# Performance work log

Hardware: AMD Instinct MI355X
Metric: run time of the kernel (lower is better)

## Reference

```python
import jax, jax.numpy as jnp
import numpy as np

B, T, DMODEL = 8, 1024, 1024
N_HEADS, DK, DV = 16, 64, 64
FF_INNER = 4096


def setup_inputs() -> dict:
    key = jax.random.key(0)
    ks = jax.random.split(key, 9)
    s = 0.02  # init scale so softmax logits stay sane
    return {
        "x": jax.random.normal(ks[0], (B, T, DMODEL), dtype=jnp.float32),
        "Wq": jax.random.normal(ks[1], (N_HEADS, DMODEL, DK), dtype=jnp.float32) * s,
        "Wk": jax.random.normal(ks[2], (N_HEADS, DMODEL, DK), dtype=jnp.float32) * s,
        "Wv": jax.random.normal(ks[3], (N_HEADS, DMODEL, DV), dtype=jnp.float32) * s,
        "Wo": jax.random.normal(ks[4], (DMODEL, DMODEL), dtype=jnp.float32) * s,
        "W1": jax.random.normal(ks[5], (FF_INNER, DMODEL), dtype=jnp.float32) * s,
        "b1": jax.random.normal(ks[6], (FF_INNER,), dtype=jnp.float32) * s,
        "W2": jax.random.normal(ks[7], (DMODEL, FF_INNER), dtype=jnp.float32) * s,
        "b2": jax.random.normal(ks[8], (DMODEL,), dtype=jnp.float32) * s,
    }


def _pseudo_norm(y):
    # Original: y - mean - std (unbiased std, torch default). NOT a real layernorm.
    mean = jnp.mean(y, axis=-1, keepdims=True)
    std = jnp.std(y, axis=-1, keepdims=True, ddof=1)
    return y - mean - std


def reference(x, Wq, Wk, Wv, Wo, W1, b1, W2, b2):
    dk = Wq.shape[-1]
    # per-head projections: (B,T,D) x (H,D,dk) -> (B,H,T,dk)
    WQ = jnp.einsum("btd,hdk->bhtk", x, Wq)
    WK = jnp.einsum("btd,hdk->bhtk", x, Wk)
    WV = jnp.einsum("btd,hdv->bhtv", x, Wv)
    scores = jnp.einsum("bhqk,bhsk->bhqs", WQ, WK) / np.sqrt(dk).astype(np.float32)
    # Faithful to original: softmax over dim=2, i.e. the QUERY axis of (B,H,Tq,Tk)
    attn = jax.nn.softmax(scores, axis=2)
    part = jnp.einsum("bhqs,bhsv->bhqv", attn, WV)  # (B,H,T,dv)
    # concat heads: (B,T,H*dv) == (B,T,dmodel)
    part = part.transpose(0, 2, 1, 3).reshape(part.shape[0], part.shape[2], -1)
    out1 = part @ Wo + x
    out1 = _pseudo_norm(out1)
    # FeedForward: Linear(dmodel->inner), relu, Linear(inner->dmodel)
    h = jnp.maximum(out1 @ W1.T + b1, 0.0)
    out2 = h @ W2.T + b2 + out1
    return _pseudo_norm(out2)
```

## Files before the change

kernel.cpp:

```cpp
#include <hip/hip_runtime.h>
#include <hip/hip_bf16.h>
#include <math.h>


#define B_ 8
#define T_ 1024
#define D_ 1024
#define H_ 16
#define DK_ 64
#define FF_ 4096
#define M_ (B_ * T_)

typedef unsigned short u16;
typedef __attribute__((ext_vector_type(8))) short bf16x8;
typedef __attribute__((ext_vector_type(4))) float f32x4;

#define QSZ 8388608ull

__device__ __forceinline__ float b2f(u16 u) {
  union { unsigned int i; float f; } x;
  x.i = ((unsigned int)u) << 16;
  return x.f;
}
__device__ __forceinline__ u16 f2b(float f) {
  __hip_bfloat16 h = __float2bfloat16(f);
  return *(u16*)&h;
}
__device__ __forceinline__ float fexp2(float x) {
#if __has_builtin(__builtin_amdgcn_exp2f)
  return __builtin_amdgcn_exp2f(x);
#else
  return exp2f(x);
#endif
}
#define C_QK 0.1803368801111244f

typedef __attribute__((address_space(1))) const void gas_void;
typedef __attribute__((address_space(3))) void las_void;
__device__ __forceinline__ void gload16(const void* g, void* l) {
  __builtin_amdgcn_global_load_lds((gas_void*)g, (las_void*)l, 16, 0, 0);
}

template <int EPI>
__global__ __launch_bounds__(256) void gemm16_k(
    const u16* __restrict__ A, const u16* __restrict__ Bt,
    int M, int N, int K, int lda, int ldb,
    float* __restrict__ C, int ldc, u16* __restrict__ Cb,
    const float* __restrict__ res, const float* __restrict__ bias) {
  __shared__ __align__(16) u16 As[2][128 * 32];
  __shared__ __align__(16) u16 Bs[2][128 * 32];

  const int tid = threadIdx.x;
  const int lane = tid & 63, wv = tid >> 6;
  const int m0 = blockIdx.y * 128, n0 = blockIdx.x * 128;
  const int wr = (wv >> 1) * 64, wc = (wv & 1) * 64;

  f32x4 acc[4][4];
#pragma unroll
  for (int i = 0; i < 4; ++i)
#pragma unroll
    for (int j = 0; j < 4; ++j) acc[i][j] = (f32x4){0.f, 0.f, 0.f, 0.f};

  const int srow = wv * 16 + (lane >> 2);
  const int scol = (lane & 3) * 8;
  const int fr = lane & 15, fk = (lane >> 4) * 8;

  const u16* gA0 = &A[(size_t)(m0 + srow) * lda + scol];
  const u16* gA1 = &A[(size_t)(m0 + srow + 64) * lda + scol];
  const u16* gB0 = &Bt[(size_t)(n0 + srow) * ldb + scol];
  const u16* gB1 = &Bt[(size_t)(n0 + srow + 64) * ldb + scol];

  gload16(gA0, &As[0][wv * 512]);
  gload16(gA1, &As[0][2048 + wv * 512]);
  gload16(gB0, &Bs[0][wv * 512]);
  gload16(gB1, &Bs[0][2048 + wv * 512]);
  __syncthreads();

  int cur = 0;
  for (int k0 = 0; k0 < K; k0 += 32) {
    if (k0 + 32 < K) {
      int nx = cur ^ 1, ko = k0 + 32;
      gload16(gA0 + ko, &As[nx][wv * 512]);
      gload16(gA1 + ko, &As[nx][2048 + wv * 512]);
      gload16(gB0 + ko, &Bs[nx][wv * 512]);
      gload16(gB1 + ko, &Bs[nx][2048 + wv * 512]);
    }
    bf16x8 af[4], bfr[4];
#pragma unroll
    for (int mi = 0; mi < 4; ++mi)
      af[mi] = *(const bf16x8*)&As[cur][(wr + mi * 16 + fr) * 32 + fk];
#pragma unroll
    for (int ni = 0; ni < 4; ++ni)
      bfr[ni] = *(const bf16x8*)&Bs[cur][(wc + ni * 16 + fr) * 32 + fk];
#pragma unroll
    for (int mi = 0; mi < 4; ++mi)
#pragma unroll
      for (int ni = 0; ni < 4; ++ni)
        acc[mi][ni] = __builtin_amdgcn_mfma_f32_16x16x32_bf16(
            af[mi], bfr[ni], acc[mi][ni], 0, 0, 0);
    __syncthreads();
    cur ^= 1;
  }

  const int fq = (lane >> 4) * 4;
#pragma unroll
  for (int mi = 0; mi < 4; ++mi) {
#pragma unroll
    for (int ni = 0; ni < 4; ++ni) {
      const int row = m0 + wr + mi * 16 + fq;
      const int col = n0 + wc + ni * 16 + fr;
      f32x4 v = acc[mi][ni];
      if (EPI == 6) {
        const int seg = col >> 10, cl = col & 1023;
        if (seg < 2) {
          u16* dst = Cb + (size_t)seg * QSZ;
#pragma unroll
          for (int r = 0; r < 4; ++r)
            dst[(size_t)(row + r) * 1024 + cl] = f2b(v[r]);
        } else {
          ushort4 w;
          w.x = f2b(v[0]); w.y = f2b(v[1]); w.z = f2b(v[2]); w.w = f2b(v[3]);
          size_t vidx = 2 * QSZ +
                        (((size_t)(row >> 10) * 16 + (cl >> 6)) * 64 +
                         (cl & 63)) * (size_t)T_ + (row & 1023);
          *(ushort4*)&Cb[vidx] = w;
        }
      } else {
#pragma unroll
        for (int r = 0; r < 4; ++r) {
          float val = v[r];
          size_t idx = (size_t)(row + r) * ldc + col;
          if (EPI == 1) {
            C[idx] = val + res[idx];
          } else if (EPI == 2) {
            Cb[idx] = f2b(fmaxf(val + bias[col], 0.f));
          } else if (EPI == 3) {
            C[idx] = val + bias[col] + res[idx];
          } else if (EPI == 4) {
            C[idx] = C[idx] + val;
          }
        }
      }
    }
  }
}

__global__ __launch_bounds__(256) void cvt_k(const float* __restrict__ in,
                                             u16* __restrict__ out, int n4) {
  int i = blockIdx.x * 256 + threadIdx.x;
  if (i >= n4) return;
  float4 v = *(const float4*)&in[(size_t)i * 4];
  ushort4 o;
  o.x = f2b(v.x); o.y = f2b(v.y); o.z = f2b(v.z); o.w = f2b(v.w);
  *(ushort4*)&out[(size_t)i * 4] = o;
}

__global__ __launch_bounds__(256) void tconv_k(const float* __restrict__ src,
                                               u16* __restrict__ dst, int R,
                                               int C) {
  __shared__ __align__(16) float t[32][33];
  const size_t bo = (size_t)blockIdx.z * R * C;
  const int r0 = blockIdx.y * 32, c0 = blockIdx.x * 32;
  const int tid = threadIdx.x;
  const int row = tid >> 3, c4 = (tid & 7) * 4;
  float4 v = *(const float4*)&src[bo + (size_t)(r0 + row) * C + c0 + c4];
  t[row][c4 + 0] = v.x; t[row][c4 + 1] = v.y;
  t[row][c4 + 2] = v.z; t[row][c4 + 3] = v.w;
  __syncthreads();
  ushort4 o;
  o.x = f2b(t[c4 + 0][row]); o.y = f2b(t[c4 + 1][row]);
  o.z = f2b(t[c4 + 2][row]); o.w = f2b(t[c4 + 3][row]);
  *(ushort4*)&dst[bo + (size_t)(c0 + row) * R + r0 + c4] = o;
}

__global__ __launch_bounds__(256) void attn_lsum_k(
    const u16* __restrict__ q, const u16* __restrict__ k,
    float* __restrict__ Lrcp) {
  __shared__ __align__(16) u16 Qs[128 * 64];
  __shared__ float Lsh[2][128];
  const int tid = threadIdx.x, lane = tid & 63, wv = tid >> 6;
  const int s0 = blockIdx.x * 128, h = blockIdx.y, b = blockIdx.z;
  const int bh = b * H_ + h;
  const u16* qbase = q + (size_t)b * T_ * D_ + h * DK_;
  const u16* kbase = k + (size_t)b * T_ * D_ + h * DK_;

  const int wr = (wv >> 1) * 64, wc = (wv & 1) * 64;
  const int fr = lane & 15, fs8 = (lane >> 4) * 8, fq = (lane >> 4) * 4;

  bf16x8 kf[4][2];
#pragma unroll
  for (int mi = 0; mi < 4; ++mi)
#pragma unroll
    for (int ks = 0; ks < 2; ++ks)
      kf[mi][ks] = *(const bf16x8*)&kbase[(size_t)(s0 + wr + mi * 16 + fr) * D_ +
                                          ks * 32 + fs8];

  float lrun[4][4];
#pragma unroll
  for (int mi = 0; mi < 4; ++mi)
#pragma unroll
    for (int r = 0; r < 4; ++r) lrun[mi][r] = 0.f;

  const int srow = wv * 8 + (lane >> 3);
  const int sscol = ((lane & 7) ^ ((lane >> 3) & 7)) * 8;

  for (int q0 = 0; q0 < T_; q0 += 128) {
    __syncthreads();
#pragma unroll
    for (int it = 0; it < 4; ++it)
      gload16(&qbase[(size_t)(q0 + it * 32 + srow) * D_ + sscol],
              &Qs[(it * 32 + wv * 8) * 64]);
    __syncthreads();

    f32x4 acc[4][4];
#pragma unroll
    for (int mi = 0; mi < 4; ++mi)
#pragma unroll
      for (int ni = 0; ni < 4; ++ni) acc[mi][ni] = (f32x4){0.f, 0.f, 0.f, 0.f};

#pragma unroll
    for (int ks = 0; ks < 2; ++ks) {
      bf16x8 qf[4];
#pragma unroll
      for (int ni = 0; ni < 4; ++ni) {
        int qr = wc + ni * 16 + fr;
        int slot = (ks * 4 + (lane >> 4)) ^ (qr & 7);
        qf[ni] = *(const bf16x8*)&Qs[qr * 64 + slot * 8];
      }
#pragma unroll
      for (int mi = 0; mi < 4; ++mi)
#pragma unroll
        for (int ni = 0; ni < 4; ++ni)
          acc[mi][ni] = __builtin_amdgcn_mfma_f32_16x16x32_bf16(
              kf[mi][ks], qf[ni], acc[mi][ni], 0, 0, 0);
    }
#pragma unroll
    for (int mi = 0; mi < 4; ++mi)
#pragma unroll
      for (int r = 0; r < 4; ++r) {
        float e = 0.f;
#pragma unroll
        for (int ni = 0; ni < 4; ++ni) e += fexp2(acc[mi][ni][r] * C_QK);
        lrun[mi][r] += e;
      }
  }

#pragma unroll
  for (int mi = 0; mi < 4; ++mi)
#pragma unroll
    for (int r = 0; r < 4; ++r) {
      float s = lrun[mi][r];
      s += __shfl_xor(s, 1, 64); s += __shfl_xor(s, 2, 64);
      s += __shfl_xor(s, 4, 64); s += __shfl_xor(s, 8, 64);
      if (fr == 0) Lsh[wv & 1][wr + mi * 16 + fq + r] = s;
    }
  __syncthreads();
  if (tid < 128)
    Lrcp[(size_t)bh * T_ + s0 + tid] = 1.f / (Lsh[0][tid] + Lsh[1][tid]);
}

__global__ __launch_bounds__(256) void vscale_k(u16* __restrict__ vt,
                                                const float* __restrict__ Lrcp) {
  int i8 = blockIdx.x * 256 + threadIdx.x;
  size_t base = (size_t)i8 * 8;
  int bh = (int)(base >> 16);
  int s = (int)(base & 1023);
  float4 r0 = *(const float4*)&Lrcp[(size_t)bh * 1024 + s];
  float4 r1 = *(const float4*)&Lrcp[(size_t)bh * 1024 + s + 4];
  ushort4 a = *(const ushort4*)&vt[base];
  ushort4 c = *(const ushort4*)&vt[base + 4];
  ushort4 oa, oc;
  oa.x = f2b(b2f(a.x) * r0.x); oa.y = f2b(b2f(a.y) * r0.y);
  oa.z = f2b(b2f(a.z) * r0.z); oa.w = f2b(b2f(a.w) * r0.w);
  oc.x = f2b(b2f(c.x) * r1.x); oc.y = f2b(b2f(c.y) * r1.y);
  oc.z = f2b(b2f(c.z) * r1.z); oc.w = f2b(b2f(c.w) * r1.w);
  *(ushort4*)&vt[base] = oa;
  *(ushort4*)&vt[base + 4] = oc;
}

__global__ __launch_bounds__(256) void attn_pv_k(
    const u16* __restrict__ q, const u16* __restrict__ k,
    const u16* __restrict__ vt, u16* __restrict__ part) {
  __shared__ __align__(16) u16 Ks[128 * 64];
  __shared__ __align__(16) u16 Vs[64 * 128];
  __shared__ __align__(16) u16 Ps[128 * 128];
  const int tid = threadIdx.x, lane = tid & 63, wv = tid >> 6;
  const int q0 = blockIdx.x * 128, h = blockIdx.y, b = blockIdx.z;
  const int bh = b * H_ + h;
  const u16* qbase = q + (size_t)b * T_ * D_ + h * DK_;
  const u16* kbase = k + (size_t)b * T_ * D_ + h * DK_;
  const u16* vtb = vt + (size_t)bh * DK_ * T_;

  const int wr = (wv >> 1) * 64, wc = (wv & 1) * 64;
  const int fr = lane & 15, fs8 = (lane >> 4) * 8, fq = (lane >> 4) * 4;

  bf16x8 qf[4][2];
#pragma unroll
  for (int ni = 0; ni < 4; ++ni)
#pragma unroll
    for (int ks = 0; ks < 2; ++ks)
      qf[ni][ks] = *(const bf16x8*)&qbase[(size_t)(q0 + wc + ni * 16 + fr) * D_ +
                                          ks * 32 + fs8];

  f32x4 acc2[2][4];
#pragma unroll
  for (int i = 0; i < 2; ++i)
#pragma unroll
    for (int j = 0; j < 4; ++j) acc2[i][j] = (f32x4){0.f, 0.f, 0.f, 0.f};

  const int ksrow = wv * 8 + (lane >> 3);
  const int kscol = ((lane & 7) ^ ((lane >> 3) & 7)) * 8;

  for (int s0 = 0; s0 < T_; s0 += 128) {
    __syncthreads();
#pragma unroll
    for (int it = 0; it < 4; ++it)
      gload16(&kbase[(size_t)(s0 + it * 32 + ksrow) * D_ + kscol],
              &Ks[(it * 32 + wv * 8) * 64]);
#pragma unroll
    for (int it = 0; it < 4; ++it) {
      int v = it * 16 + wv * 4 + (lane >> 4);
      int sslot = (lane & 15) ^ (v & 7);
      gload16(&vtb[(size_t)v * T_ + s0 + sslot * 8],
              &Vs[(it * 16 + wv * 4) * 128]);
    }
    __syncthreads();

    f32x4 st[4][4];
#pragma unroll
    for (int mi = 0; mi < 4; ++mi)
#pragma unroll
      for (int ni = 0; ni < 4; ++ni) st[mi][ni] = (f32x4){0.f, 0.f, 0.f, 0.f};
#pragma unroll
    for (int ks = 0; ks < 2; ++ks) {
      bf16x8 kfa[4];
#pragma unroll
      for (int mi = 0; mi < 4; ++mi) {
        int sr = wr + mi * 16 + fr;
        int slot = (ks * 4 + (lane >> 4)) ^ (sr & 7);
        kfa[mi] = *(const bf16x8*)&Ks[sr * 64 + slot * 8];
      }
#pragma unroll
      for (int mi = 0; mi < 4; ++mi)
#pragma unroll
        for (int ni = 0; ni < 4; ++ni)
          st[mi][ni] = __builtin_amdgcn_mfma_f32_16x16x32_bf16(
              kfa[mi], qf[ni][ks], st[mi][ni], 0, 0, 0);
    }

#pragma unroll
    for (int ni = 0; ni < 4; ++ni) {
      int qcol = wc + ni * 16 + fr;
#pragma unroll
      for (int mi = 0; mi < 4; ++mi) {
        int sb = wr + mi * 16 + fq;
        u16 e0 = f2b(fexp2(st[mi][ni][0] * C_QK));
        u16 e1 = f2b(fexp2(st[mi][ni][1] * C_QK));
        u16 e2 = f2b(fexp2(st[mi][ni][2] * C_QK));
        u16 e3 = f2b(fexp2(st[mi][ni][3] * C_QK));
        uint2 w;
        w.x = (unsigned int)e0 | ((unsigned int)e1 << 16);
        w.y = (unsigned int)e2 | ((unsigned int)e3 << 16);
        int byte = qcol * 256 + ((sb * 2) ^ ((qcol & 15) << 4));
        *(uint2*)((char*)Ps + byte) = w;
      }
    }
    __syncthreads();

#pragma unroll
    for (int ks2 = 0; ks2 < 4; ++ks2) {
      bf16x8 pa[2], vb2[4];
#pragma unroll
      for (int mi2 = 0; mi2 < 2; ++mi2) {
        int qr = wv * 32 + mi2 * 16 + fr;
        int byte = qr * 256 + (((ks2 * 32 + (lane >> 4) * 8) * 2) ^ ((qr & 15) << 4));
        pa[mi2] = *(const bf16x8*)((const char*)Ps + byte);
      }
#pragma unroll
      for (int ni2 = 0; ni2 < 4; ++ni2) {
        int v = ni2 * 16 + fr;
        int slot = (ks2 * 4 + (lane >> 4)) ^ (v & 7);
        vb2[ni2] = *(const bf16x8*)&Vs[v * 128 + slot * 8];
      }
#pragma unroll
      for (int mi2 = 0; mi2 < 2; ++mi2)
#pragma unroll
        for (int ni2 = 0; ni2 < 4; ++ni2)
          acc2[mi2][ni2] = __builtin_amdgcn_mfma_f32_16x16x32_bf16(
              pa[mi2], vb2[ni2], acc2[mi2][ni2], 0, 0, 0);
    }
  }

#pragma unroll
  for (int mi2 = 0; mi2 < 2; ++mi2)
#pragma unroll
    for (int ni2 = 0; ni2 < 4; ++ni2)
#pragma unroll
      for (int r = 0; r < 4; ++r) {
        int qrow = q0 + wv * 32 + mi2 * 16 + fq + r;
        int v = ni2 * 16 + fr;
        part[(size_t)(b * T_ + qrow) * D_ + h * DK_ + v] =
            f2b(acc2[mi2][ni2][r]);
      }
}

template <bool WB>
__global__ __launch_bounds__(256) void norm_k(const float* __restrict__ in,
                                              float* __restrict__ out,
                                              u16* __restrict__ ob) {
  __shared__ float red[8];
  const int row = blockIdx.x, tid = threadIdx.x;
  float4 vv = *(const float4*)&in[(size_t)row * D_ + tid * 4];
  float s = vv.x + vv.y + vv.z + vv.w;
  for (int off = 1; off < 64; off <<= 1) s += __shfl_xor(s, off, 64);
  if ((tid & 63) == 0) red[tid >> 6] = s;
  __syncthreads();
  float mean = (red[0] + red[1] + red[2] + red[3]) * (1.f / 1024.f);
  float dx = vv.x - mean, dy = vv.y - mean, dz = vv.z - mean, dw = vv.w - mean;
  float s2 = dx * dx + dy * dy + dz * dz + dw * dw;
  __syncthreads();
  for (int off = 1; off < 64; off <<= 1) s2 += __shfl_xor(s2, off, 64);
  if ((tid & 63) == 0) red[4 + (tid >> 6)] = s2;
  __syncthreads();
  float var = (red[4] + red[5] + red[6] + red[7]) * (1.f / 1023.f);
  float sd = sqrtf(var);
  float4 o = {dx - sd, dy - sd, dz - sd, dw - sd};
  *(float4*)&out[(size_t)row * D_ + tid * 4] = o;
  if (WB) {
    ushort4 q;
    q.x = f2b(o.x); q.y = f2b(o.y); q.z = f2b(o.z); q.w = f2b(o.w);
    *(ushort4*)&ob[(size_t)row * D_ + tid * 4] = q;
  }
}

extern "C" void kernel_launch(void* const* d_in, const int* in_sizes, int n_in,
                              void* d_out, int out_size, void* d_ws,
                              size_t ws_size, hipStream_t stream) {
  const float* x  = (const float*)d_in[0];
  const float* Wq = (const float*)d_in[1];
  const float* Wk = (const float*)d_in[2];
  const float* Wv = (const float*)d_in[3];
  const float* Wo = (const float*)d_in[4];
  const float* W1 = (const float*)d_in[5];
  const float* b1 = (const float*)d_in[6];
  const float* W2 = (const float*)d_in[7];
  const float* b2 = (const float*)d_in[8];

  char* w = (char*)d_ws;
  u16* qb16   = (u16*)(w + (0ull << 20));
  u16* kb16   = (u16*)(w + (16ull << 20));
  u16* Vt     = (u16*)(w + (32ull << 20));
  u16* xb     = (u16*)(w + (48ull << 20));
  u16* part16 = (u16*)(w + (64ull << 20));
  u16* Wqkv   = (u16*)(w + (80ull << 20));
  u16* Wot    = (u16*)(w + (86ull << 20));
  u16* W1b    = (u16*)(w + (88ull << 20));
  u16* W2b    = (u16*)(w + (96ull << 20));
  float* Lrcp = (float*)(w + (104ull << 20));
  u16* o1b = qb16;
  u16* hc  = kb16;
  float* o1 = (float*)d_out;

  dim3 thr(256);

  int n4x = (M_ * D_) / 4;
  cvt_k<<<dim3((n4x + 255) / 256), thr, 0, stream>>>(x, xb, n4x);
  tconv_k<<<dim3(2, 32, 16), thr, 0, stream>>>(Wq, Wqkv, 1024, 64);
  tconv_k<<<dim3(2, 32, 16), thr, 0, stream>>>(Wk, Wqkv + 1048576, 1024, 64);
  tconv_k<<<dim3(2, 32, 16), thr, 0, stream>>>(Wv, Wqkv + 2097152, 1024, 64);
  tconv_k<<<dim3(32, 32, 1), thr, 0, stream>>>(Wo, Wot, 1024, 1024);
  int n4w = (FF_ * D_) / 4;
  cvt_k<<<dim3((n4w + 255) / 256), thr, 0, stream>>>(W1, W1b, n4w);
  cvt_k<<<dim3((n4w + 255) / 256), thr, 0, stream>>>(W2, W2b, n4w);

  gemm16_k<6><<<dim3(3072 / 128, M_ / 128), thr, 0, stream>>>(
      xb, Wqkv, M_, 3072, D_, D_, D_, nullptr, D_, qb16, nullptr, nullptr);

  dim3 ga(T_ / 128, H_, B_);
  attn_lsum_k<<<ga, thr, 0, stream>>>(qb16, kb16, Lrcp);
  vscale_k<<<dim3((int)(QSZ / 8 / 256)), thr, 0, stream>>>(Vt, Lrcp);
  attn_pv_k<<<ga, thr, 0, stream>>>(qb16, kb16, Vt, part16);

  gemm16_k<1><<<dim3(D_ / 128, M_ / 128), thr, 0, stream>>>(
      part16, Wot, M_, D_, D_, D_, D_, o1, D_, nullptr, x, nullptr);
  norm_k<true><<<dim3(M_), thr, 0, stream>>>(o1, o1, o1b);

  for (int c = 0; c < 2; ++c) {
    const u16* W1c = W1b + (size_t)c * 2048 * 1024;
    const u16* W2c = W2b + (size_t)c * 2048;
    gemm16_k<2><<<dim3(2048 / 128, M_ / 128), thr, 0, stream>>>(
        o1b, W1c, M_, 2048, 1024, 1024, 1024, nullptr, 2048, hc, nullptr,
        b1 + c * 2048);
    if (c == 0) {
      gemm16_k<3><<<dim3(D_ / 128, M_ / 128), thr, 0, stream>>>(
          hc, W2c, M_, 1024, 2048, 2048, FF_, o1, D_, nullptr, o1, b2);
    } else {
      gemm16_k<4><<<dim3(D_ / 128, M_ / 128), thr, 0, stream>>>(
          hc, W2c, M_, 1024, 2048, 2048, FF_, o1, D_, nullptr, nullptr, nullptr);
    }
  }

  norm_k<false><<<dim3(M_), thr, 0, stream>>>(o1, o1, nullptr);
}
```

Baseline: 613.3 us.

## Swizzle GEMM blocks and LDS layout, and run the FFN as one unchunked pass

The GEMM kernel now uses a 1D grid and remaps block indices in strides of 8, aiming to place neighbouring tiles on the same XCD for better L2 reuse. The LDS tile columns are XOR-swizzled on both the global-to-LDS store and the fragment reads to reduce bank conflicts. The two-chunk FFN loop is replaced by a single W1 GEMM over the full 4096 inner width and a single W2 GEMM with K=4096. This removes the read-modify-write accumulate epilogue and one extra pass over the output. The trade-off is a larger hidden-activation buffer, which must fit in the workspace without overlapping live buffers, and the block swizzle assumes the grid size is a multiple of 8.

After: 556.3 us. -9.3%, faster.

```diff
diff --git a/kernel.cpp b/kernel.cpp
--- a/kernel.cpp
+++ b/kernel.cpp
@@ -44,7 +44,7 @@
 template <int EPI>
 __global__ __launch_bounds__(256) void gemm16_k(
     const u16* __restrict__ A, const u16* __restrict__ Bt,
-    int M, int N, int K, int lda, int ldb,
+    int M, int N, int K, int lda, int ldb, int nbx,
     float* __restrict__ C, int ldc, u16* __restrict__ Cb,
     const float* __restrict__ res, const float* __restrict__ bias) {
   __shared__ __align__(16) u16 As[2][128 * 32];
@@ -52,7 +52,11 @@
 
   const int tid = threadIdx.x;
   const int lane = tid & 63, wv = tid >> 6;
-  const int m0 = blockIdx.y * 128, n0 = blockIdx.x * 128;
+
+  const int nwg = (int)gridDim.x;
+  const int sw = (blockIdx.x & 7) * (nwg >> 3) + (blockIdx.x >> 3);
+  const int m0 = (sw / nbx) * 128, n0 = (sw % nbx) * 128;
+
   const int wr = (wv >> 1) * 64, wc = (wv & 1) * 64;
 
   f32x4 acc[4][4];
@@ -62,8 +66,8 @@
     for (int j = 0; j < 4; ++j) acc[i][j] = (f32x4){0.f, 0.f, 0.f, 0.f};
 
   const int srow = wv * 16 + (lane >> 2);
-  const int scol = (lane & 3) * 8;
-  const int fr = lane & 15, fk = (lane >> 4) * 8;
+  const int scol = ((lane & 3) ^ ((lane >> 2) & 3)) * 8;
+  const int fr = lane & 15, fj = lane >> 4;
 
   const u16* gA0 = &A[(size_t)(m0 + srow) * lda + scol];
   const u16* gA1 = &A[(size_t)(m0 + srow + 64) * lda + scol];
@@ -87,11 +91,15 @@
     }
     bf16x8 af[4], bfr[4];
 #pragma unroll
-    for (int mi = 0; mi < 4; ++mi)
-      af[mi] = *(const bf16x8*)&As[cur][(wr + mi * 16 + fr) * 32 + fk];
-#pragma unroll
-    for (int ni = 0; ni < 4; ++ni)
-      bfr[ni] = *(const bf16x8*)&Bs[cur][(wc + ni * 16 + fr) * 32 + fk];
+    for (int mi = 0; mi < 4; ++mi) {
+      int row = wr + mi * 16 + fr;
+      af[mi] = *(const bf16x8*)&As[cur][row * 32 + ((fj ^ (fr & 3)) * 8)];
+    }
+#pragma unroll
+    for (int ni = 0; ni < 4; ++ni) {
+      int row = wc + ni * 16 + fr;
+      bfr[ni] = *(const bf16x8*)&Bs[cur][row * 32 + ((fj ^ (fr & 3)) * 8)];
+    }
 #pragma unroll
     for (int mi = 0; mi < 4; ++mi)
 #pragma unroll
@@ -136,8 +144,6 @@
             Cb[idx] = f2b(fmaxf(val + bias[col], 0.f));
           } else if (EPI == 3) {
             C[idx] = val + bias[col] + res[idx];
-          } else if (EPI == 4) {
-            C[idx] = C[idx] + val;
           }
         }
       }
@@ -473,32 +479,24 @@
   cvt_k<<<dim3((n4w + 255) / 256), thr, 0, stream>>>(W1, W1b, n4w);
   cvt_k<<<dim3((n4w + 255) / 256), thr, 0, stream>>>(W2, W2b, n4w);
 
-  gemm16_k<6><<<dim3(3072 / 128, M_ / 128), thr, 0, stream>>>(
-      xb, Wqkv, M_, 3072, D_, D_, D_, nullptr, D_, qb16, nullptr, nullptr);
+  gemm16_k<6><<<dim3((3072 / 128) * (M_ / 128)), thr, 0, stream>>>(
+      xb, Wqkv, M_, 3072, D_, D_, D_, 3072 / 128, nullptr, D_, qb16,
+      nullptr, nullptr);
 
   dim3 ga(T_ / 128, H_, B_);
   attn_lsum_k<<<ga, thr, 0, stream>>>(qb16, kb16, Lrcp);
   vscale_k<<<dim3((int)(QSZ / 8 / 256)), thr, 0, stream>>>(Vt, Lrcp);
   attn_pv_k<<<ga, thr, 0, stream>>>(qb16, kb16, Vt, part16);
 
-  gemm16_k<1><<<dim3(D_ / 128, M_ / 128), thr, 0, stream>>>(
-      part16, Wot, M_, D_, D_, D_, D_, o1, D_, nullptr, x, nullptr);
+  gemm16_k<1><<<dim3((D_ / 128) * (M_ / 128)), thr, 0, stream>>>(
+      part16, Wot, M_, D_, D_, D_, D_, D_ / 128, o1, D_, nullptr, x, nullptr);
   norm_k<true><<<dim3(M_), thr, 0, stream>>>(o1, o1, o1b);
 
-  for (int c = 0; c < 2; ++c) {
-    const u16* W1c = W1b + (size_t)c * 2048 * 1024;
-    const u16* W2c = W2b + (size_t)c * 2048;
-    gemm16_k<2><<<dim3(2048 / 128, M_ / 128), thr, 0, stream>>>(
-        o1b, W1c, M_, 2048, 1024, 1024, 1024, nullptr, 2048, hc, nullptr,
-        b1 + c * 2048);
-    if (c == 0) {
-      gemm16_k<3><<<dim3(D_ / 128, M_ / 128), thr, 0, stream>>>(
-          hc, W2c, M_, 1024, 2048, 2048, FF_, o1, D_, nullptr, o1, b2);
-    } else {
-      gemm16_k<4><<<dim3(D_ / 128, M_ / 128), thr, 0, stream>>>(
-          hc, W2c, M_, 1024, 2048, 2048, FF_, o1, D_, nullptr, nullptr, nullptr);
-    }
-  }
+  gemm16_k<2><<<dim3((FF_ / 128) * (M_ / 128)), thr, 0, stream>>>(
+      o1b, W1b, M_, FF_, D_, D_, D_, FF_ / 128, nullptr, FF_, hc,
+      nullptr, b1);
+  gemm16_k<3><<<dim3((D_ / 128) * (M_ / 128)), thr, 0, stream>>>(
+      hc, W2b, M_, D_, FF_, FF_, FF_, D_ / 128, o1, D_, nullptr, o1, b2);
 
   norm_k<false><<<dim3(M_), thr, 0, stream>>>(o1, o1, nullptr);
 }
```
